# Kernel tuning notes

Hardware: AMD Instinct MI355X
Metric: run time of the kernel (lower is better)

## Reference

```python
import jax, jax.numpy as jnp
import numpy as np

B, T, D, H, V = 512, 128, 1024, 1024, 256
STEPS = 26  # batch_max_length (25) + 1


def setup_inputs() -> dict:
    key = jax.random.key(0)
    ks = jax.random.split(key, 12)
    s = lambda *sh: 1.0 / np.sqrt(sh[-1])
    inp = {
        "batch_H": jax.random.normal(ks[0], (B, T, D), dtype=jnp.float32),
        "text": jax.random.randint(ks[1], (B, STEPS), 0, V, dtype=jnp.int64),
        # AttentionCell params
        "i2h_w": jax.random.normal(ks[2], (H, D), dtype=jnp.float32) * s(H, D),
        "h2h_w": jax.random.normal(ks[3], (H, H), dtype=jnp.float32) * s(H, H),
        "h2h_b": jnp.zeros((H,), dtype=jnp.float32),
        "score_w": jax.random.normal(ks[4], (1, H), dtype=jnp.float32) * s(1, H),
        # LSTMCell params (input = context[D] ++ onehot[V])
        "W_ih": jax.random.normal(ks[5], (4 * H, D + V), dtype=jnp.float32) * s(4 * H, D + V),
        "W_hh": jax.random.normal(ks[6], (4 * H, H), dtype=jnp.float32) * s(4 * H, H),
        "b_ih": jnp.zeros((4 * H,), dtype=jnp.float32),
        "b_hh": jnp.zeros((4 * H,), dtype=jnp.float32),
        # generator
        "gen_w": jax.random.normal(ks[7], (V, H), dtype=jnp.float32) * s(V, H),
        "gen_b": jnp.zeros((V,), dtype=jnp.float32),
    }
    return inp


def reference(batch_H, text, i2h_w, h2h_w, h2h_b, score_w, W_ih, W_hh, b_ih, b_hh, gen_w, gen_b):
    # proj_H = i2h(batch_H): step-invariant, hoisted out of the loop (same math)
    proj_H = jnp.einsum("btd,hd->bth", batch_H, i2h_w)  # [B,T,H]
    dtype = batch_H.dtype

    def step(carry, tok):
        h, c = carry
        # Bahdanau additive attention
        proj_h = h @ h2h_w.T + h2h_b                       # [B,H]
        e = jnp.tanh(proj_H + proj_h[:, None, :]) @ score_w[0]  # [B,T]
        alpha = jax.nn.softmax(e, axis=1)                   # [B,T]
        context = jnp.einsum("bt,btd->bd", alpha, batch_H)  # [B,D]
        x = jnp.concatenate([context, jax.nn.one_hot(tok, V, dtype=dtype)], axis=1)
        # LSTMCell (torch gate order: i, f, g, o)
        gates = x @ W_ih.T + b_ih + h @ W_hh.T + b_hh       # [B,4H]
        i_g, f_g, g_g, o_g = jnp.split(gates, 4, axis=1)
        c_new = jax.nn.sigmoid(f_g) * c + jax.nn.sigmoid(i_g) * jnp.tanh(g_g)
        h_new = jax.nn.sigmoid(o_g) * jnp.tanh(c_new)
        return (h_new, c_new), h_new

    h0 = jnp.zeros((B, H), dtype=dtype)
    c0 = jnp.zeros((B, H), dtype=dtype)
    tokens = jnp.swapaxes(text[:, :STEPS], 0, 1)            # [STEPS,B]
    _, out_hid = jax.lax.scan(step, (h0, c0), tokens)       # [STEPS,B,H]
    out_hid = jnp.swapaxes(out_hid, 0, 1)                   # [B,STEPS,H]
    logits = jnp.einsum("bsh,vh->bsv", out_hid, gen_w) + gen_b
    return logits  # [B, STEPS, V]
```

## Files before the change

kernel.cpp:

```cpp
#include <hip/hip_runtime.h>
#include <hip/hip_fp16.h>

#define BB 512
#define TT 128
#define DD 1024
#define HH 1024
#define VV 256
#define SS 26

typedef _Float16 half8 __attribute__((ext_vector_type(8)));
typedef _Float16 half4 __attribute__((ext_vector_type(4)));
typedef float f32x4 __attribute__((ext_vector_type(4)));

__device__ __forceinline__ void cp16(const void* g, void* l) {
    __builtin_amdgcn_global_load_lds(
        (const __attribute__((address_space(1))) void*)g,
        (__attribute__((address_space(3))) void*)l, 16, 0, 0);
}

__device__ __forceinline__ float tanh_fast(float x) {
    float ex = __expf(2.f * x);
    return 1.f - 2.f * __builtin_amdgcn_rcpf(ex + 1.f);
}
__device__ __forceinline__ float sigmoid_fast(float x) {
    return __builtin_amdgcn_rcpf(1.f + __expf(-x));
}

__global__ void cvt_f32_to_f16_v4(const float* __restrict__ src,
                                  _Float16* __restrict__ dst, long n4) {
    long i = (long)blockIdx.x * blockDim.x + threadIdx.x;
    long stride = (long)gridDim.x * blockDim.x;
    for (; i < n4; i += stride) {
        float4 v = ((const float4*)src)[i];
        half4 h;
        h[0] = (_Float16)v.x; h[1] = (_Float16)v.y;
        h[2] = (_Float16)v.z; h[3] = (_Float16)v.w;
        ((half4*)dst)[i] = h;
    }
}

__global__ void build_wcatp(const float* __restrict__ W_ih,
                            const float* __restrict__ W_hh,
                            _Float16* __restrict__ wcatp) {
    int idx = blockIdx.x * 256 + threadIdx.x;
    int c = idx >> 11;
    int k = idx & 2047;
    int g = c >> 6, q = (c >> 4) & 3, jl = c & 15;
    int row = q * 1024 + g * 16 + jl;
    float v = (k < 1024) ? W_ih[(size_t)row * 1280 + k]
                         : W_hh[(size_t)row * 1024 + (k - 1024)];
    wcatp[idx] = (_Float16)v;
}

__global__ void build_onehT(const float* __restrict__ W_ih,
                            float* __restrict__ onehT) {
    int idx = blockIdx.x * 256 + threadIdx.x;
    int v = idx >> 12;
    int g = idx & 4095;
    onehT[idx] = W_ih[(size_t)g * 1280 + 1024 + v];
}

__global__ void build_bsum(const float* __restrict__ b_ih,
                           const float* __restrict__ b_hh,
                           float* __restrict__ bsum) {
    int i = blockIdx.x * 256 + threadIdx.x;
    bsum[i] = b_ih[i] + b_hh[i];
}

template <int MODE, int SWZ>
__global__ __launch_bounds__(256) void gemm_bt(
    const _Float16* __restrict__ A, int lda,
    const _Float16* __restrict__ B, int ldb,
    void* __restrict__ Cp, int ldc, int K, const float* __restrict__ bias) {
    __shared__ __align__(16) _Float16 As[128 * 32];
    __shared__ __align__(16) _Float16 Bs[128 * 32];

    int bx = blockIdx.x, by = blockIdx.y;
    if (SWZ) {
        int nx = gridDim.x;
        int bid = by * nx + bx;
        int xcd = bid & 7;
        int local = bid >> 3;
        int rows_per_xcd = gridDim.y >> 3;
        bx = local % nx;
        by = xcd * rows_per_xcd + local / nx;
    }
    const int tid  = threadIdx.x;
    const int lane = tid & 63;
    const int wid  = tid >> 6;
    const int wm   = wid >> 1;
    const int wn   = wid & 1;
    const int m0 = by * 128;
    const int n0 = bx * 128;

    f32x4 acc[4][4];
#pragma unroll
    for (int i = 0; i < 4; ++i)
#pragma unroll
        for (int j = 0; j < 4; ++j)
            acc[i][j] = (f32x4){0.f, 0.f, 0.f, 0.f};

    const int row0 = tid >> 2;
    const int ch0  = tid & 3;
    const _Float16* a0 = A + (size_t)(m0 + row0) * lda + ch0 * 8;
    const _Float16* a1 = A + (size_t)(m0 + row0 + 64) * lda + ch0 * 8;
    const _Float16* b0 = B + (size_t)(n0 + row0) * ldb + ch0 * 8;
    const _Float16* b1 = B + (size_t)(n0 + row0 + 64) * ldb + ch0 * 8;
    _Float16* sa0 = As + tid * 8;
    _Float16* sa1 = As + 64 * 32 + tid * 8;
    _Float16* sb0 = Bs + tid * 8;
    _Float16* sb1 = Bs + 64 * 32 + tid * 8;

    const int la = lane & 15;
    const int kc = (lane >> 4) * 8;

    for (int k0 = 0; k0 < K; k0 += 32) {
        __syncthreads();
        cp16(a0 + k0, sa0);
        cp16(a1 + k0, sa1);
        cp16(b0 + k0, sb0);
        cp16(b1 + k0, sb1);
        __syncthreads();

        half8 af[4], bf[4];
#pragma unroll
        for (int mt = 0; mt < 4; ++mt)
            af[mt] = *(const half8*)(As + (wm * 64 + mt * 16 + la) * 32 + kc);
#pragma unroll
        for (int nt = 0; nt < 4; ++nt)
            bf[nt] = *(const half8*)(Bs + (wn * 64 + nt * 16 + la) * 32 + kc);
#pragma unroll
        for (int mt = 0; mt < 4; ++mt)
#pragma unroll
            for (int nt = 0; nt < 4; ++nt)
                acc[mt][nt] = __builtin_amdgcn_mfma_f32_16x16x32_f16(
                    af[mt], bf[nt], acc[mt][nt], 0, 0, 0);
    }

#pragma unroll
    for (int mt = 0; mt < 4; ++mt) {
#pragma unroll
        for (int nt = 0; nt < 4; ++nt) {
            int gn = n0 + wn * 64 + nt * 16 + la;
            float bv = bias ? bias[gn] : 0.f;
#pragma unroll
            for (int r = 0; r < 4; ++r) {
                int gm = m0 + wm * 64 + mt * 16 + (lane >> 4) * 4 + r;
                float v = acc[mt][nt][r] + bv;
                if (MODE == 1) {
                    ((_Float16*)Cp)[(size_t)gm * ldc + gn] = (_Float16)v;
                } else {
                    int s = gm >> 9;
                    int b = gm & 511;
                    ((float*)Cp)[((size_t)b * SS + s) * VV + gn] = v;
                }
            }
        }
    }
}

#define GEMM64_CORE(A, lda, B, ldb, K)                                        \
    __shared__ __align__(16) _Float16 As[64 * 32];                            \
    __shared__ __align__(16) _Float16 Bs[128 * 32];                           \
    const int tid  = threadIdx.x;                                             \
    const int lane = tid & 63;                                                \
    const int wid  = tid >> 6;                                                \
    const int wm   = wid >> 1;                                                \
    const int wn   = wid & 1;                                                 \
    const int m0 = blockIdx.y * 64;                                           \
    const int n0 = blockIdx.x * 128;                                          \
    f32x4 acc[2][4];                                                          \
    _Pragma("unroll") for (int i = 0; i < 2; ++i)                             \
        _Pragma("unroll") for (int j = 0; j < 4; ++j)                         \
            acc[i][j] = (f32x4){0.f, 0.f, 0.f, 0.f};                          \
    const int row0 = tid >> 2;                                                \
    const int ch0  = tid & 3;                                                 \
    const _Float16* ag  = A + (size_t)(m0 + row0) * lda + ch0 * 8;            \
    const _Float16* bg0 = B + (size_t)(n0 + row0) * ldb + ch0 * 8;            \
    const _Float16* bg1 = B + (size_t)(n0 + row0 + 64) * ldb + ch0 * 8;       \
    _Float16* sa  = As + tid * 8;                                             \
    _Float16* sb0 = Bs + tid * 8;                                             \
    _Float16* sb1 = Bs + 64 * 32 + tid * 8;                                   \
    const int la = lane & 15;                                                 \
    const int kc = (lane >> 4) * 8;                                           \
    for (int k0 = 0; k0 < K; k0 += 32) {                                      \
        __syncthreads();                                                      \
        cp16(ag + k0, sa);                                                    \
        cp16(bg0 + k0, sb0);                                                  \
        cp16(bg1 + k0, sb1);                                                  \
        __syncthreads();                                                      \
        half8 af[2], bf[4];                                                   \
        _Pragma("unroll") for (int mt = 0; mt < 2; ++mt)                      \
            af[mt] = *(const half8*)(As + (wm * 32 + mt * 16 + la) * 32 + kc);\
        _Pragma("unroll") for (int nt = 0; nt < 4; ++nt)                      \
            bf[nt] = *(const half8*)(Bs + (wn * 64 + nt * 16 + la) * 32 + kc);\
        _Pragma("unroll") for (int mt = 0; mt < 2; ++mt)                      \
            _Pragma("unroll") for (int nt = 0; nt < 4; ++nt)                  \
                acc[mt][nt] = __builtin_amdgcn_mfma_f32_16x16x32_f16(         \
                    af[mt], bf[nt], acc[mt][nt], 0, 0, 0);                    \
    }

__global__ __launch_bounds__(256) void gemm64_f32(
    const _Float16* __restrict__ A, int lda,
    const _Float16* __restrict__ B, int ldb,
    float* __restrict__ C, int ldc, int K, const float* __restrict__ bias) {
    GEMM64_CORE(A, lda, B, ldb, K)
#pragma unroll
    for (int mt = 0; mt < 2; ++mt)
#pragma unroll
        for (int nt = 0; nt < 4; ++nt) {
            int gn = n0 + wn * 64 + nt * 16 + la;
            float bv = bias[gn];
#pragma unroll
            for (int r = 0; r < 4; ++r) {
                int gm = m0 + wm * 32 + mt * 16 + (lane >> 4) * 4 + r;
                C[(size_t)gm * ldc + gn] = acc[mt][nt][r] + bv;
            }
        }
}

__global__ __launch_bounds__(256) void gemm_gates(
    const _Float16* __restrict__ A,
    const _Float16* __restrict__ B,
    const float* __restrict__ bsum,
    const float* __restrict__ onehT,
    const int* __restrict__ text,
    int step,
    float* __restrict__ c,
    _Float16* __restrict__ acat,
    _Float16* __restrict__ hid) {
    GEMM64_CORE(A, 2048, B, 2048, 2048)
    const int quad = lane >> 4;
    const int jb = (n0 >> 2) + wn * 16 + la;
    float bs[4];
#pragma unroll
    for (int q = 0; q < 4; ++q) bs[q] = bsum[q * 1024 + jb];
#pragma unroll
    for (int mt = 0; mt < 2; ++mt) {
#pragma unroll
        for (int r = 0; r < 4; ++r) {
            int b = m0 + wm * 32 + mt * 16 + quad * 4 + r;
            int tok = text[b * SS + step];
            const float* orow = onehT + (size_t)tok * 4096;
            float ig = acc[mt][0][r] + bs[0] + orow[jb];
            float fg = acc[mt][1][r] + bs[1] + orow[1024 + jb];
            float gg = acc[mt][2][r] + bs[2] + orow[2048 + jb];
            float og = acc[mt][3][r] + bs[3] + orow[3072 + jb];
            size_t ci = (size_t)b * 1024 + jb;
            float cn = sigmoid_fast(fg) * c[ci] + sigmoid_fast(ig) * tanh_fast(gg);
            float hn = sigmoid_fast(og) * tanh_fast(cn);
            c[ci] = cn;
            _Float16 h16 = (_Float16)hn;
            acat[(size_t)b * 2048 + 1024 + jb] = h16;
            hid[((size_t)step * BB + b) * HH + jb] = h16;
        }
    }
}

__global__ __launch_bounds__(512) void attn_kernel(
    const _Float16* __restrict__ pH,
    const _Float16* __restrict__ bh,
    const float* __restrict__ ph,
    const float* __restrict__ sw,
    _Float16* __restrict__ acat) {
    __shared__ float e_s[TT];
    __shared__ float al_s[TT];
    __shared__ __align__(16) float pc[2][DD];

    const int b = blockIdx.x;
    const int tid = threadIdx.x;
    const int lane = tid & 63;
    const int wv = tid >> 6;

    float phr[16], swr[16];
    const float4* ph4 = (const float4*)(ph + (size_t)b * HH + lane * 16);
    const float4* sw4 = (const float4*)(sw + lane * 16);
#pragma unroll
    for (int q = 0; q < 4; ++q) {
        float4 t1 = ph4[q];
        phr[q * 4 + 0] = t1.x; phr[q * 4 + 1] = t1.y;
        phr[q * 4 + 2] = t1.z; phr[q * 4 + 3] = t1.w;
        float4 t2 = sw4[q];
        swr[q * 4 + 0] = t2.x; swr[q * 4 + 1] = t2.y;
        swr[q * 4 + 2] = t2.z; swr[q * 4 + 3] = t2.w;
    }

    const _Float16* pHb = pH + (size_t)b * TT * HH + lane * 16;
    for (int tt = 0; tt < 16; ++tt) {
        int t = wv * 16 + tt;
        half8 p0 = *(const half8*)(pHb + (size_t)t * HH);
        half8 p1 = *(const half8*)(pHb + (size_t)t * HH + 8);
        float acc = 0.f;
#pragma unroll
        for (int k = 0; k < 8; ++k)
            acc += tanh_fast((float)p0[k] + phr[k]) * swr[k];
#pragma unroll
        for (int k = 0; k < 8; ++k)
            acc += tanh_fast((float)p1[k] + phr[8 + k]) * swr[8 + k];
#pragma unroll
        for (int off = 32; off > 0; off >>= 1) acc += __shfl_xor(acc, off, 64);
        if (lane == 0) e_s[t] = acc;
    }
    __syncthreads();

    if (tid < TT) {
        float m = -1e30f;
        for (int t = 0; t < TT; ++t) m = fmaxf(m, e_s[t]);
        float s = 0.f;
        for (int t = 0; t < TT; ++t) s += __expf(e_s[t] - m);
        al_s[tid] = __expf(e_s[tid] - m) / s;
    }
    __syncthreads();

    const int w2 = tid >> 8;
    const int lc = tid & 255;
    const _Float16* bhb = bh + (size_t)b * TT * DD + lc * 4;
    float c0 = 0.f, c1 = 0.f, c2 = 0.f, c3 = 0.f;
#pragma unroll 4
    for (int t = w2 * 64; t < w2 * 64 + 64; ++t) {
        float a = al_s[t];
        half4 v = *(const half4*)(bhb + (size_t)t * DD);
        c0 += a * (float)v[0];
        c1 += a * (float)v[1];
        c2 += a * (float)v[2];
        c3 += a * (float)v[3];
    }
    ((float4*)pc[w2])[lc] = make_float4(c0, c1, c2, c3);
    __syncthreads();

    if (tid < 256) {
        float4 x0 = ((const float4*)pc[0])[tid];
        float4 x1 = ((const float4*)pc[1])[tid];
        half4 o;
        o[0] = (_Float16)(x0.x + x1.x);
        o[1] = (_Float16)(x0.y + x1.y);
        o[2] = (_Float16)(x0.z + x1.z);
        o[3] = (_Float16)(x0.w + x1.w);
        *(half4*)(acat + (size_t)b * 2048 + tid * 4) = o;
    }
}

extern "C" void kernel_launch(void* const* d_in, const int* in_sizes, int n_in,
                              void* d_out, int out_size, void* d_ws, size_t ws_size,
                              hipStream_t stream) {
    const float* batch_H = (const float*)d_in[0];
    const int*   text    = (const int*)d_in[1];
    const float* i2h_w   = (const float*)d_in[2];
    const float* h2h_w   = (const float*)d_in[3];
    const float* h2h_b   = (const float*)d_in[4];
    const float* score_w = (const float*)d_in[5];
    const float* W_ih    = (const float*)d_in[6];
    const float* W_hh    = (const float*)d_in[7];
    const float* b_ih    = (const float*)d_in[8];
    const float* b_hh    = (const float*)d_in[9];
    const float* gen_w   = (const float*)d_in[10];
    const float* gen_b   = (const float*)d_in[11];
    float* out = (float*)d_out;

    char* ws = (char*)d_ws;
    size_t off = 0;
    auto carve = [&](size_t bytes) -> void* {
        void* p = ws + off;
        off += (bytes + 255) & ~(size_t)255;
        return p;
    };
    _Float16* bh16   = (_Float16*)carve((size_t)BB * TT * DD * 2);
    _Float16* pH16   = (_Float16*)carve((size_t)BB * TT * HH * 2);
    _Float16* wi2h16 = (_Float16*)carve((size_t)HH * DD * 2);
    _Float16* wh2h16 = (_Float16*)carve((size_t)HH * HH * 2);
    _Float16* wcatp  = (_Float16*)carve((size_t)4 * HH * 2048 * 2);
    _Float16* wgen16 = (_Float16*)carve((size_t)VV * HH * 2);
    float*    onehT  = (float*)carve((size_t)VV * 4 * HH * 4);
    float*    bsum   = (float*)carve((size_t)4 * HH * 4);
    _Float16* acat   = (_Float16*)carve((size_t)BB * 2048 * 2);
    float*    ph_f   = (float*)carve((size_t)BB * HH * 4);
    float*    c_f    = (float*)carve((size_t)BB * HH * 4);
    _Float16* hid16  = (_Float16*)carve((size_t)SS * BB * HH * 2);

    const dim3 blk(256);

    cvt_f32_to_f16_v4<<<dim3(16384), blk, 0, stream>>>(batch_H, bh16, (long)BB * TT * DD / 4);
    cvt_f32_to_f16_v4<<<dim3(1024), blk, 0, stream>>>(i2h_w, wi2h16, (long)HH * DD / 4);
    cvt_f32_to_f16_v4<<<dim3(1024), blk, 0, stream>>>(h2h_w, wh2h16, (long)HH * HH / 4);
    cvt_f32_to_f16_v4<<<dim3(256), blk, 0, stream>>>(gen_w, wgen16, (long)VV * HH / 4);
    build_wcatp<<<dim3(4 * HH * 2048 / 256), blk, 0, stream>>>(W_ih, W_hh, wcatp);
    build_onehT<<<dim3(VV * 4 * HH / 256), blk, 0, stream>>>(W_ih, onehT);
    build_bsum<<<dim3(16), blk, 0, stream>>>(b_ih, b_hh, bsum);
    hipMemsetAsync(acat, 0, (size_t)BB * 2048 * 2, stream);
    hipMemsetAsync(c_f, 0, (size_t)BB * HH * 4, stream);

    gemm_bt<1, 1><<<dim3(HH / 128, BB * TT / 128), blk, 0, stream>>>(
        bh16, DD, wi2h16, DD, pH16, HH, DD, nullptr);

    for (int s = 0; s < SS; ++s) {
        gemm64_f32<<<dim3(HH / 128, BB / 64), blk, 0, stream>>>(
            acat + 1024, 2048, wh2h16, HH, ph_f, HH, HH, h2h_b);

        attn_kernel<<<dim3(BB), dim3(512), 0, stream>>>(pH16, bh16, ph_f, score_w, acat);

        gemm_gates<<<dim3(4 * HH / 128, BB / 64), blk, 0, stream>>>(
            acat, wcatp, bsum, onehT, text, s, c_f, acat, hid16);
    }

    gemm_bt<2, 0><<<dim3(VV / 128, SS * BB / 128), blk, 0, stream>>>(
        hid16, HH, wgen16, HH, out, VV, HH, gen_b);
}
```

Before: 3.577 ms.

## Double-buffer GEMM LDS tiles, retile h2h GEMM, split i2h GEMM launches

```diff
diff --git a/kernel.cpp b/kernel.cpp
--- a/kernel.cpp
+++ b/kernel.cpp
@@ -72,8 +72,8 @@
     const _Float16* __restrict__ A, int lda,
     const _Float16* __restrict__ B, int ldb,
     void* __restrict__ Cp, int ldc, int K, const float* __restrict__ bias) {
-    __shared__ __align__(16) _Float16 As[128 * 32];
-    __shared__ __align__(16) _Float16 Bs[128 * 32];
+    __shared__ __align__(16) _Float16 As[2][128 * 32];
+    __shared__ __align__(16) _Float16 Bs[2][128 * 32];
 
     int bx = blockIdx.x, by = blockIdx.y;
     if (SWZ) {
@@ -106,35 +106,41 @@
     const _Float16* a1 = A + (size_t)(m0 + row0 + 64) * lda + ch0 * 8;
     const _Float16* b0 = B + (size_t)(n0 + row0) * ldb + ch0 * 8;
     const _Float16* b1 = B + (size_t)(n0 + row0 + 64) * ldb + ch0 * 8;
-    _Float16* sa0 = As + tid * 8;
-    _Float16* sa1 = As + 64 * 32 + tid * 8;
-    _Float16* sb0 = Bs + tid * 8;
-    _Float16* sb1 = Bs + 64 * 32 + tid * 8;
 
     const int la = lane & 15;
     const int kc = (lane >> 4) * 8;
 
-    for (int k0 = 0; k0 < K; k0 += 32) {
-        __syncthreads();
-        cp16(a0 + k0, sa0);
-        cp16(a1 + k0, sa1);
-        cp16(b0 + k0, sb0);
-        cp16(b1 + k0, sb1);
-        __syncthreads();
-
+    auto stage = [&](int buf, int k0) {
+        cp16(a0 + k0, &As[buf][tid * 8]);
+        cp16(a1 + k0, &As[buf][64 * 32 + tid * 8]);
+        cp16(b0 + k0, &Bs[buf][tid * 8]);
+        cp16(b1 + k0, &Bs[buf][64 * 32 + tid * 8]);
+    };
+    auto compute = [&](int buf) {
         half8 af[4], bf[4];
 #pragma unroll
         for (int mt = 0; mt < 4; ++mt)
-            af[mt] = *(const half8*)(As + (wm * 64 + mt * 16 + la) * 32 + kc);
+            af[mt] = *(const half8*)(&As[buf][(wm * 64 + mt * 16 + la) * 32 + kc]);
 #pragma unroll
         for (int nt = 0; nt < 4; ++nt)
-            bf[nt] = *(const half8*)(Bs + (wn * 64 + nt * 16 + la) * 32 + kc);
+            bf[nt] = *(const half8*)(&Bs[buf][(wn * 64 + nt * 16 + la) * 32 + kc]);
 #pragma unroll
         for (int mt = 0; mt < 4; ++mt)
 #pragma unroll
             for (int nt = 0; nt < 4; ++nt)
                 acc[mt][nt] = __builtin_amdgcn_mfma_f32_16x16x32_f16(
                     af[mt], bf[nt], acc[mt][nt], 0, 0, 0);
+    };
+
+    stage(0, 0);
+    __syncthreads();
+    for (int k0 = 0; k0 < K; k0 += 64) {
+        stage(1, k0 + 32);
+        compute(0);
+        __syncthreads();
+        if (k0 + 64 < K) stage(0, k0 + 64);
+        compute(1);
+        __syncthreads();
     }
 
 #pragma unroll
@@ -159,64 +165,52 @@
     }
 }
 
-#define GEMM64_CORE(A, lda, B, ldb, K)                                        \
-    __shared__ __align__(16) _Float16 As[64 * 32];                            \
-    __shared__ __align__(16) _Float16 Bs[128 * 32];                           \
-    const int tid  = threadIdx.x;                                             \
-    const int lane = tid & 63;                                                \
-    const int wid  = tid >> 6;                                                \
-    const int wm   = wid >> 1;                                                \
-    const int wn   = wid & 1;                                                 \
-    const int m0 = blockIdx.y * 64;                                           \
-    const int n0 = blockIdx.x * 128;                                          \
-    f32x4 acc[2][4];                                                          \
-    _Pragma("unroll") for (int i = 0; i < 2; ++i)                             \
-        _Pragma("unroll") for (int j = 0; j < 4; ++j)                         \
-            acc[i][j] = (f32x4){0.f, 0.f, 0.f, 0.f};                          \
-    const int row0 = tid >> 2;                                                \
-    const int ch0  = tid & 3;                                                 \
-    const _Float16* ag  = A + (size_t)(m0 + row0) * lda + ch0 * 8;            \
-    const _Float16* bg0 = B + (size_t)(n0 + row0) * ldb + ch0 * 8;            \
-    const _Float16* bg1 = B + (size_t)(n0 + row0 + 64) * ldb + ch0 * 8;       \
-    _Float16* sa  = As + tid * 8;                                             \
-    _Float16* sb0 = Bs + tid * 8;                                             \
-    _Float16* sb1 = Bs + 64 * 32 + tid * 8;                                   \
-    const int la = lane & 15;                                                 \
-    const int kc = (lane >> 4) * 8;                                           \
-    for (int k0 = 0; k0 < K; k0 += 32) {                                      \
-        __syncthreads();                                                      \
-        cp16(ag + k0, sa);                                                    \
-        cp16(bg0 + k0, sb0);                                                  \
-        cp16(bg1 + k0, sb1);                                                  \
-        __syncthreads();                                                      \
-        half8 af[2], bf[4];                                                   \
-        _Pragma("unroll") for (int mt = 0; mt < 2; ++mt)                      \
-            af[mt] = *(const half8*)(As + (wm * 32 + mt * 16 + la) * 32 + kc);\
-        _Pragma("unroll") for (int nt = 0; nt < 4; ++nt)                      \
-            bf[nt] = *(const half8*)(Bs + (wn * 64 + nt * 16 + la) * 32 + kc);\
-        _Pragma("unroll") for (int mt = 0; mt < 2; ++mt)                      \
-            _Pragma("unroll") for (int nt = 0; nt < 4; ++nt)                  \
-                acc[mt][nt] = __builtin_amdgcn_mfma_f32_16x16x32_f16(         \
-                    af[mt], bf[nt], acc[mt][nt], 0, 0, 0);                    \
-    }
-
-__global__ __launch_bounds__(256) void gemm64_f32(
+__global__ __launch_bounds__(256) void gemm_ph(
     const _Float16* __restrict__ A, int lda,
     const _Float16* __restrict__ B, int ldb,
     float* __restrict__ C, int ldc, int K, const float* __restrict__ bias) {
-    GEMM64_CORE(A, lda, B, ldb, K)
-#pragma unroll
-    for (int mt = 0; mt < 2; ++mt)
-#pragma unroll
-        for (int nt = 0; nt < 4; ++nt) {
-            int gn = n0 + wn * 64 + nt * 16 + la;
-            float bv = bias[gn];
-#pragma unroll
-            for (int r = 0; r < 4; ++r) {
-                int gm = m0 + wm * 32 + mt * 16 + (lane >> 4) * 4 + r;
-                C[(size_t)gm * ldc + gn] = acc[mt][nt][r] + bv;
-            }
-        }
+    __shared__ __align__(16) _Float16 As[2][16 * 32];
+    __shared__ __align__(16) _Float16 Bs[2][64 * 32];
+    const int tid  = threadIdx.x;
+    const int lane = tid & 63;
+    const int wid  = tid >> 6;
+    const int m0 = blockIdx.y * 16;
+    const int n0 = blockIdx.x * 64;
+    const int row = tid >> 2;
+    const int ch  = tid & 3;
+    const _Float16* ag = A + (size_t)(m0 + (row & 15)) * lda + ch * 8;
+    const _Float16* bg = B + (size_t)(n0 + row) * ldb + ch * 8;
+    f32x4 acc = (f32x4){0.f, 0.f, 0.f, 0.f};
+    const int la = lane & 15;
+    const int kc = (lane >> 4) * 8;
+
+    auto stage = [&](int buf, int k0) {
+        if (tid < 64) cp16(ag + k0, &As[buf][tid * 8]);
+        cp16(bg + k0, &Bs[buf][tid * 8]);
+    };
+    auto compute = [&](int buf) {
+        half8 af = *(const half8*)(&As[buf][la * 32 + kc]);
+        half8 bf = *(const half8*)(&Bs[buf][(wid * 16 + la) * 32 + kc]);
+        acc = __builtin_amdgcn_mfma_f32_16x16x32_f16(af, bf, acc, 0, 0, 0);
+    };
+
+    stage(0, 0);
+    __syncthreads();
+    for (int k0 = 0; k0 < K; k0 += 64) {
+        stage(1, k0 + 32);
+        compute(0);
+        __syncthreads();
+        if (k0 + 64 < K) stage(0, k0 + 64);
+        compute(1);
+        __syncthreads();
+    }
+
+    int gn = n0 + wid * 16 + la;
+    float bv = bias[gn];
+    int gm0 = m0 + (lane >> 4) * 4;
+#pragma unroll
+    for (int r = 0; r < 4; ++r)
+        C[(size_t)(gm0 + r) * ldc + gn] = acc[r] + bv;
 }
 
 __global__ __launch_bounds__(256) void gemm_gates(
@@ -229,7 +223,64 @@
     float* __restrict__ c,
     _Float16* __restrict__ acat,
     _Float16* __restrict__ hid) {
-    GEMM64_CORE(A, 2048, B, 2048, 2048)
+    __shared__ __align__(16) _Float16 As[2][64 * 32];
+    __shared__ __align__(16) _Float16 Bs[2][128 * 32];
+    const int tid  = threadIdx.x;
+    const int lane = tid & 63;
+    const int wid  = tid >> 6;
+    const int wm   = wid >> 1;
+    const int wn   = wid & 1;
+    const int m0 = blockIdx.y * 64;
+    const int n0 = blockIdx.x * 128;
+    const int K  = 2048;
+
+    f32x4 acc[2][4];
+#pragma unroll
+    for (int i = 0; i < 2; ++i)
+#pragma unroll
+        for (int j = 0; j < 4; ++j)
+            acc[i][j] = (f32x4){0.f, 0.f, 0.f, 0.f};
+
+    const int row0 = tid >> 2;
+    const int ch0  = tid & 3;
+    const _Float16* ag  = A + (size_t)(m0 + row0) * 2048 + ch0 * 8;
+    const _Float16* bg0 = B + (size_t)(n0 + row0) * 2048 + ch0 * 8;
+    const _Float16* bg1 = B + (size_t)(n0 + row0 + 64) * 2048 + ch0 * 8;
+    const int la = lane & 15;
+    const int kc = (lane >> 4) * 8;
+
+    auto stage = [&](int buf, int k0) {
+        cp16(ag + k0, &As[buf][tid * 8]);
+        cp16(bg0 + k0, &Bs[buf][tid * 8]);
+        cp16(bg1 + k0, &Bs[buf][64 * 32 + tid * 8]);
+    };
+    auto compute = [&](int buf) {
+        half8 af[2], bf[4];
+#pragma unroll
+        for (int mt = 0; mt < 2; ++mt)
+            af[mt] = *(const half8*)(&As[buf][(wm * 32 + mt * 16 + la) * 32 + kc]);
+#pragma unroll
+        for (int nt = 0; nt < 4; ++nt)
+            bf[nt] = *(const half8*)(&Bs[buf][(wn * 64 + nt * 16 + la) * 32 + kc]);
+#pragma unroll
+        for (int mt = 0; mt < 2; ++mt)
+#pragma unroll
+            for (int nt = 0; nt < 4; ++nt)
+                acc[mt][nt] = __builtin_amdgcn_mfma_f32_16x16x32_f16(
+                    af[mt], bf[nt], acc[mt][nt], 0, 0, 0);
+    };
+
+    stage(0, 0);
+    __syncthreads();
+    for (int k0 = 0; k0 < K; k0 += 64) {
+        stage(1, k0 + 32);
+        compute(0);
+        __syncthreads();
+        if (k0 + 64 < K) stage(0, k0 + 64);
+        compute(1);
+        __syncthreads();
+    }
+
     const int quad = lane >> 4;
     const int jb = (n0 >> 2) + wn * 16 + la;
     float bs[4];
@@ -286,6 +337,7 @@
     }
 
     const _Float16* pHb = pH + (size_t)b * TT * HH + lane * 16;
+#pragma unroll 2
     for (int tt = 0; tt < 16; ++tt) {
         int t = wv * 16 + tt;
         half8 p0 = *(const half8*)(pHb + (size_t)t * HH);
@@ -316,7 +368,7 @@
     const int lc = tid & 255;
     const _Float16* bhb = bh + (size_t)b * TT * DD + lc * 4;
     float c0 = 0.f, c1 = 0.f, c2 = 0.f, c3 = 0.f;
-#pragma unroll 4
+#pragma unroll 8
     for (int t = w2 * 64; t < w2 * 64 + 64; ++t) {
         float a = al_s[t];
         half4 v = *(const half4*)(bhb + (size_t)t * DD);
@@ -389,11 +441,14 @@
     hipMemsetAsync(acat, 0, (size_t)BB * 2048 * 2, stream);
     hipMemsetAsync(c_f, 0, (size_t)BB * HH * 4, stream);
 
-    gemm_bt<1, 1><<<dim3(HH / 128, BB * TT / 128), blk, 0, stream>>>(
-        bh16, DD, wi2h16, DD, pH16, HH, DD, nullptr);
+    for (int i = 0; i < 8; ++i) {
+        gemm_bt<1, 1><<<dim3(HH / 128, BB * TT / 128 / 8), blk, 0, stream>>>(
+            bh16 + (size_t)i * (BB * TT / 8) * DD, DD, wi2h16, DD,
+            pH16 + (size_t)i * (BB * TT / 8) * HH, HH, DD, nullptr);
+    }
 
     for (int s = 0; s < SS; ++s) {
-        gemm64_f32<<<dim3(HH / 128, BB / 64), blk, 0, stream>>>(
+        gemm_ph<<<dim3(HH / 64, BB / 16), blk, 0, stream>>>(
             acat + 1024, 2048, wh2h16, HH, ph_f, HH, HH, h2h_b);
 
         attn_kernel<<<dim3(BB), dim3(512), 0, stream>>>(pH16, bh16, ph_f, score_w, acat);
```

Measured after the change: 3.606 ms. About the same (+0.8%).
